# Kernel tuning notes

Measured on AMD Instinct MI355X. Metric: run time of the kernel, lower is better.

Reference implementation:

```python
import jax, jax.numpy as jnp
import numpy as np
from jax.scipy.special import erf, digamma, i0

B, L, D, H = 4, 4096, 512, 4
_MAX_SQRT_GRADIENT = 1000.0

@jax.custom_vjp
def sqrt_bound(x):
    return jnp.sqrt(x)

def _sb_fwd(x):
    return jnp.sqrt(x), x

def _sb_bwd(x, g):
    return (g / jnp.sqrt(jnp.clip(4.0 * x, 1.0 / _MAX_SQRT_GRADIENT**2, None)),)

sqrt_bound.defvjp(_sb_fwd, _sb_bwd)

def block_diag_linear(x, w):
    # x: [..., D], w: [h, bw, bw] block-diagonal weight
    h, bw, _ = w.shape
    xr = x.reshape(x.shape[:-1] + (h, bw))
    return jnp.einsum('...hi,hij->...hj', xr, w).reshape(x.shape)

def self_att_pool(x, num_heads):
    n_state = x.shape[-1] // num_heads
    attn = jax.nn.softmax(jnp.einsum('bld,bmd->blm', x, x) / np.float32(np.sqrt(n_state)), axis=-1)
    # max over the sequence axis of the attended values, keepdims -> [B,1,D]
    return jnp.max(jnp.einsum('blm,bmd->bld', attn, x), axis=-2, keepdims=True)

def ripple_transform_hybrid(t, mix_params):
    mix = jax.nn.softmax(mix_params)
    return mix[0] * digamma(t + 1.0) + mix[1] * i0(t)

def ripple_act(data, alpha, beta, mix_params, temperature=1.0):
    def f(d):
        norm = erf(d / (jnp.max(d) * alpha))
        return jnp.sum(ripple_transform_hybrid(norm * beta, mix_params))
    g = jnp.clip(jax.grad(f)(data), -1.0, 1.0)
    return jax.nn.softmax(-g / temperature, axis=-1)  # softmin

def ripplemoe_act(data, weights, alphas, beta, mix_params, temperature=1.0):
    def f(d):
        dmax = jnp.max(d)
        norm = erf(d[None] / (dmax * alphas[:, None, None]))  # [S,B,L]
        t = ripple_transform_hybrid(norm * beta, mix_params)
        w = jax.nn.softmax(weights)
        return jnp.sum(w[:, None, None] * t)
    g = jnp.clip(jax.grad(f)(data), -1.0, 1.0)
    return jax.nn.softmax(-g / temperature, axis=-1)  # softmin

def token_selection(x, cls_w, cls_b, token_weights, prelu_a, ts_weights, ts_alphas, ts_beta, ts_mix):
    scores = jnp.einsum('bld,sd->sbl', x, cls_w) + cls_b[:, None, None]  # [S,B,L]
    p = jnp.where(scores >= 0, scores, prelu_a * scores)  # PReLU
    ts = jax.nn.celu(p) * jax.nn.silu(p) + jax.nn.gelu(p, approximate=False)
    combined = jnp.einsum('s,sbl->bl', jax.nn.selu(token_weights[:, 0]), ts)
    _, idx = jax.lax.top_k(combined, combined.shape[-1])  # k = L, descending permutation
    vals = ts.sum(0)  # [B,L]
    b_idx = jnp.arange(combined.shape[0])[:, None]
    importance = jnp.ones_like(combined).at[b_idx, idx].add(vals)
    return (1.0 + ripplemoe_act(importance, ts_weights, ts_alphas, ts_beta, ts_mix))[..., None]

def _forward(x, attention_space, W_spatial, W_sil, W_ohead, W_out, w_ig, w_ag, a_param,
             cls_w, cls_b, token_weights, prelu_a, ts_weights, ts_alphas, ts_beta, ts_mix,
             pa1_alpha, pa1_beta, pa1_mix, pa2_alpha, pa2_beta, pa2_mix):
    spatial = jnp.einsum('bld,de->ble', x, attention_space) @ W_spatial.T
    # RG-LRU style gating
    gate_x = jax.nn.sigmoid(block_diag_linear(x, w_ig))
    gate_a = jax.nn.sigmoid(block_diag_linear(x, w_ag))
    log_a = -8.0 * jax.nn.softplus(a_param) * gate_a
    normalized_x = x * gate_x * sqrt_bound(1.0 - jnp.exp(2.0 * log_a))
    gated = jnp.exp(log_a) * self_att_pool(spatial, H) + normalized_x
    sparsity = ripple_act(gated @ W_sil.T, pa1_alpha, pa1_beta, pa1_mix)
    attn = (gated * sparsity) @ W_ohead.T
    sel = token_selection(x, cls_w, cls_b, token_weights, prelu_a, ts_weights, ts_alphas, ts_beta, ts_mix)
    out = ripple_act(attn * sel, pa2_alpha, pa2_beta, pa2_mix)
    return out @ W_out.T

def setup_inputs() -> dict:
    key = jax.random.key(0)
    ks = jax.random.split(key, 12)
    lim = float(1.0 / np.sqrt(D))
    xav = float(np.sqrt(6.0 / (2 * D)))
    bw = D // H
    u = jax.random.uniform(ks[8], (D,), jnp.float32, 0.9**2 + 1e-8, 0.999**2 + 1e-8)
    return {
        'x': jax.random.normal(ks[0], (B, L, D), jnp.float32),
        'attention_space': jax.random.uniform(ks[1], (D, D), jnp.float32, -xav, xav),
        'W_spatial': jax.random.uniform(ks[2], (D, D), jnp.float32, -lim, lim),
        'W_sil': jax.random.uniform(ks[3], (D, D), jnp.float32, -lim, lim),
        'W_ohead': jax.random.uniform(ks[4], (D, D), jnp.float32, -lim, lim),
        'W_out': jax.random.uniform(ks[5], (D, D), jnp.float32, -lim, lim),
        'w_ig': jax.random.normal(ks[6], (H, bw, bw), jnp.float32) * np.float32(np.sqrt(1.0 / bw)),
        'w_ag': jax.random.normal(ks[7], (H, bw, bw), jnp.float32) * np.float32(np.sqrt(1.0 / bw)),
        'a_param': jnp.log(jnp.exp(-0.5 * jnp.log(u)) - 1.0),
        'cls_w': jax.random.uniform(ks[9], (H, D), jnp.float32, -lim, lim),
        'cls_b': jax.random.uniform(ks[10], (H,), jnp.float32, -lim, lim),
        'token_weights': jax.random.normal(ks[11], (H, 1), jnp.float32),
        'prelu_a': jnp.array(0.25, jnp.float32),
        'ts_weights': jnp.ones(H, jnp.float32) / H,
        'ts_alphas': jnp.ones(H, jnp.float32),
        'ts_beta': jnp.array(1.0, jnp.float32),
        'ts_mix': jnp.full((2,), 0.5, jnp.float32),
        'pa1_alpha': jnp.array(1.0, jnp.float32),
        'pa1_beta': jnp.array(1.0, jnp.float32),
        'pa1_mix': jnp.full((2,), 0.5, jnp.float32),
        'pa2_alpha': jnp.array(1.0, jnp.float32),
        'pa2_beta': jnp.array(1.0, jnp.float32),
        'pa2_mix': jnp.full((2,), 0.5, jnp.float32),
    }

def reference(x, attention_space, W_spatial, W_sil, W_ohead, W_out, w_ig, w_ag, a_param,
              cls_w, cls_b, token_weights, prelu_a, ts_weights, ts_alphas, ts_beta, ts_mix,
              pa1_alpha, pa1_beta, pa1_mix, pa2_alpha, pa2_beta, pa2_mix):
    return _forward(x, attention_space, W_spatial, W_sil, W_ohead, W_out, w_ig, w_ag, a_param,
                    cls_w, cls_b, token_weights, prelu_a, ts_weights, ts_alphas, ts_beta, ts_mix,
                    pa1_alpha, pa1_beta, pa1_mix, pa2_alpha, pa2_beta, pa2_mix)
```

## Files before the change

kernel.cpp:

```cpp
#include <hip/hip_runtime.h>

typedef unsigned short ushort;
typedef unsigned int uint;
typedef unsigned long long u64;

#define DEV __device__ __forceinline__

typedef __attribute__((ext_vector_type(4))) float f32x4;
typedef __bf16 bf16x8 __attribute__((ext_vector_type(8)));
typedef __attribute__((ext_vector_type(4))) ushort u16x4;
typedef __attribute__((ext_vector_type(8))) ushort u16x8;

static constexpr int B_ = 4, L_ = 4096, D_ = 512;
static constexpr long NE = (long)B_ * L_ * D_;

DEV float b2f(ushort u) { return __uint_as_float(((uint)u) << 16); }
DEV ushort f2b(float f) {
    uint u = __float_as_uint(f);
    uint r = u + 0x7FFFu + ((u >> 16) & 1u);
    return (ushort)(r >> 16);
}
DEV uint mapF(float f) {
    uint b = __float_as_uint(f);
    return (b & 0x80000000u) ? ~b : (b | 0x80000000u);
}
DEV float unmapF(uint u) {
    uint b = (u & 0x80000000u) ? (u & 0x7FFFFFFFu) : ~u;
    return __uint_as_float(b);
}
DEV float rcp_(float x) { return __builtin_amdgcn_rcpf(x); }
DEV float fexp(float x) { return __builtin_amdgcn_exp2f(x * 1.44269504089f); }
DEV float sigm(float x) { return rcp_(1.f + fexp(-x)); }

DEV void gload16(const ushort* g, ushort* l) {
    __builtin_amdgcn_global_load_lds((const __attribute__((address_space(1))) void*)g,
                                     (__attribute__((address_space(3))) void*)l, 16, 0, 0);
}

DEV int xcd_swz(int b, int nwg) {
    int q = nwg >> 3, r = nwg & 7;
    int x = b & 7, i = b >> 3;
    int base = (x < r) ? x * (q + 1) : r * (q + 1) + (x - r) * q;
    return base + i;
}

DEV float trigamma1p(float t) {
    float x = t + 1.f;
    float acc = 0.f;
#pragma unroll
    for (int k = 0; k < 6; k++) { float xx = x + (float)k; acc += rcp_(xx * xx); }
    float y = x + 6.f;
    float iy = rcp_(y), iy2 = iy * iy;
    return acc + iy * (1.f + iy * (0.5f + iy * (0.166666667f + iy2 * (-0.0333333333f + iy2 * 0.0238095238f))));
}
DEV float besselI1(float t) {
    float q = 0.25f * t * t;
    return 0.5f * t * (1.f + q * (0.5f + q * (0.0833333333f + q * (0.00694444444f + q * (3.47222222e-4f + q * 1.15740741e-5f)))));
}
DEV float rippleH(float u, float beta, float mix0, float mix1) {
    float t = beta * erff(u);
    float Tp = mix0 * trigamma1p(t) + mix1 * besselI1(t);
    float ep = 1.12837917f * fexp(-u * u);
    return beta * Tp * ep;
}

DEV void gemm_core(const ushort* __restrict__ A, int lda,
                   const ushort* __restrict__ Bt, int ldb, int K,
                   ushort* __restrict__ Alds, ushort* __restrict__ Blds,
                   f32x4 (&acc)[4][4])
{
    const int tid = threadIdx.x;
    const int lane = tid & 63;
    const int wave = tid >> 6;
    const int wr = wave >> 1, wc = wave & 1;

    const int srow = wave * 16 + (lane >> 2);
    const int skc = (lane & 3) * 8;
    const ushort* Ag0 = A + (size_t)srow * lda + skc;
    const ushort* Ag1 = A + (size_t)(srow + 64) * lda + skc;
    const ushort* Bg0 = Bt + (size_t)srow * ldb + skc;
    const ushort* Bg1 = Bt + (size_t)(srow + 64) * ldb + skc;
    const int wb = wave * 512;

    const int ar = wr * 64 + (lane & 15);
    const int br = wc * 64 + (lane & 15);
    const int kk = (lane >> 4) * 8;

    gload16(Ag0, Alds + wb);
    gload16(Ag1, Alds + 2048 + wb);
    gload16(Bg0, Blds + wb);
    gload16(Bg1, Blds + 2048 + wb);
    __syncthreads();

    int cur = 0;
    for (int k0 = 0; k0 < K; k0 += 32) {
        const int nb = cur ^ 1;
        if (k0 + 32 < K) {
            gload16(Ag0 + k0 + 32, Alds + nb * 4096 + wb);
            gload16(Ag1 + k0 + 32, Alds + nb * 4096 + 2048 + wb);
            gload16(Bg0 + k0 + 32, Blds + nb * 4096 + wb);
            gload16(Bg1 + k0 + 32, Blds + nb * 4096 + 2048 + wb);
        }
        bf16x8 af[4], bfr[4];
#pragma unroll
        for (int mi = 0; mi < 4; mi++) af[mi] = *(const bf16x8*)&Alds[cur * 4096 + (ar + mi * 16) * 32 + kk];
#pragma unroll
        for (int ni = 0; ni < 4; ni++) bfr[ni] = *(const bf16x8*)&Blds[cur * 4096 + (br + ni * 16) * 32 + kk];
#pragma unroll
        for (int mi = 0; mi < 4; mi++)
#pragma unroll
            for (int ni = 0; ni < 4; ni++)
                acc[mi][ni] = __builtin_amdgcn_mfma_f32_16x16x32_bf16(af[mi], bfr[ni], acc[mi][ni], 0, 0, 0);
        __syncthreads();
        cur = nb;
    }
}

template <int MODE, bool DOMAX>
__global__ __launch_bounds__(256, 4) void gemm_bt(
    const ushort* __restrict__ A, int lda,
    const ushort* __restrict__ Bt, int ldb,
    void* __restrict__ Cv, int ldc, int K,
    const float* __restrict__ rowScale, u64* __restrict__ pmax)
{
    __shared__ ushort Alds[2 * 128 * 32];
    __shared__ ushort Blds[2 * 128 * 32];
    const int nwg = gridDim.x * gridDim.y;
    const int s = xcd_swz(blockIdx.y * gridDim.x + blockIdx.x, nwg);
    const int bx = s % gridDim.x, by = s / gridDim.x;
    const int row0 = by * 128, col0 = bx * 128;
    f32x4 acc[4][4] = {};
    gemm_core(A + (size_t)row0 * lda, lda, Bt + (size_t)col0 * ldb, ldb, K, Alds, Blds, acc);

    const int tid = threadIdx.x;
    const int lane = tid & 63;
    const int wave = tid >> 6;
    const int wr = wave >> 1, wc = wave & 1;
    const int ocol = col0 + wc * 64 + (lane & 15);
    u64 lp = 0;
#pragma unroll
    for (int mi = 0; mi < 4; mi++) {
        const int rbase = row0 + wr * 64 + mi * 16 + (lane >> 4) * 4;
#pragma unroll
        for (int j = 0; j < 4; j++) {
            float sc = (MODE == 3) ? rowScale[rbase + j] : 1.f;
#pragma unroll
            for (int ni = 0; ni < 4; ni++) {
                float v = acc[mi][ni][j] * sc;
                int cc = ocol + ni * 16;
                if (MODE == 0) ((float*)Cv)[(size_t)(rbase + j) * ldc + cc] = v;
                else ((ushort*)Cv)[(size_t)(rbase + j) * ldc + cc] = f2b(v);
                if (DOMAX) {
                    uint idx = (uint)((rbase + j) * ldc + cc);
                    u64 p = ((u64)mapF(v) << 32) | (u64)(~idx);
                    lp = (p > lp) ? p : lp;
                }
            }
        }
    }
    if (DOMAX) {
#pragma unroll
        for (int off = 32; off > 0; off >>= 1) {
            u64 o = __shfl_xor(lp, off);
            lp = (o > lp) ? o : lp;
        }
        if (lane == 0) atomicMax(pmax, lp);
    }
}

__global__ __launch_bounds__(512, 1) void gemm256_exp_k(
    const ushort* __restrict__ spP,
    ushort* __restrict__ Sout,
    float* __restrict__ rowsum)
{
    __shared__ ushort Alds[2 * 256 * 64];
    __shared__ ushort Blds[2 * 256 * 64];
    const int z = blockIdx.z;
    const int nwg = gridDim.x * gridDim.y;
    const int s = xcd_swz(blockIdx.y * gridDim.x + blockIdx.x, nwg);
    const int bx = s % gridDim.x, by = s / gridDim.x;
    const int row0 = by * 256, col0 = bx * 256;
    const ushort* A = spP + (size_t)z * (4096 * 512) + (size_t)row0 * 512;
    const ushort* Bt = spP + (size_t)z * (4096 * 512) + (size_t)col0 * 512;

    const int tid = threadIdx.x;
    const int lane = tid & 63;
    const int wave = tid >> 6;
    const int wr = wave >> 2, wc = wave & 3;

    const int lrow = lane >> 3;
    const int lchunk = (lane & 7) ^ lrow;
    const ushort* Asrc = A + (size_t)(wave * 32 + lrow) * 512 + lchunk * 8;
    const ushort* Bsrc = Bt + (size_t)(wave * 32 + lrow) * 512 + lchunk * 8;
    const int wlds = wave * 2048;

    const int ar = wr * 128 + (lane & 15);
    const int br = wc * 64 + (lane & 15);

    f32x4 acc[8][4] = {};

#define STG(kt, bf) do { \
    _Pragma("unroll") \
    for (int c = 0; c < 4; c++) { \
        gload16(Asrc + (size_t)c * 8 * 512 + (kt) * 64, Alds + (bf) * 16384 + wlds + c * 512); \
        gload16(Bsrc + (size_t)c * 8 * 512 + (kt) * 64, Blds + (bf) * 16384 + wlds + c * 512); \
    } } while (0)

    STG(0, 0);

    for (int kt = 0; kt < 8; kt++) {
        const int cb = kt & 1;
        if (kt < 7) STG(kt + 1, cb ^ 1);
        if (kt < 7) asm volatile("s_waitcnt vmcnt(8)" ::: "memory");
        else        asm volatile("s_waitcnt vmcnt(0)" ::: "memory");
        __builtin_amdgcn_s_barrier();
        asm volatile("" ::: "memory");
        __builtin_amdgcn_s_setprio(1);
#pragma unroll
        for (int ks = 0; ks < 2; ks++) {
            const int kc = ((ks * 4 + (lane >> 4)) ^ (lane & 7)) * 8;
            bf16x8 af[8], bfr[4];
#pragma unroll
            for (int mi = 0; mi < 8; mi++) af[mi] = *(const bf16x8*)&Alds[cb * 16384 + (ar + mi * 16) * 64 + kc];
#pragma unroll
            for (int ni = 0; ni < 4; ni++) bfr[ni] = *(const bf16x8*)&Blds[cb * 16384 + (br + ni * 16) * 64 + kc];
#pragma unroll
            for (int mi = 0; mi < 8; mi++)
#pragma unroll
                for (int ni = 0; ni < 4; ni++)
                    acc[mi][ni] = __builtin_amdgcn_mfma_f32_16x16x32_bf16(af[mi], bfr[ni], acc[mi][ni], 0, 0, 0);
        }
        __builtin_amdgcn_s_setprio(0);
        asm volatile("s_waitcnt lgkmcnt(0)" ::: "memory");
        __builtin_amdgcn_s_barrier();
        asm volatile("" ::: "memory");
    }
#undef STG

    ushort* C = Sout + (size_t)z * 16777216;
    float* rs = rowsum + z * 4096;
    const float sc128 = 0.0883883476f;
    const int ocol = col0 + wc * 64 + (lane & 15);
#pragma unroll
    for (int mi = 0; mi < 8; mi++) {
        const int rbase = row0 + wr * 128 + mi * 16 + (lane >> 4) * 4;
#pragma unroll
        for (int j = 0; j < 4; j++) {
            float rsum = 0.f;
#pragma unroll
            for (int ni = 0; ni < 4; ni++) {
                float p = fexp(acc[mi][ni][j] * sc128);
                C[(size_t)(rbase + j) * 4096 + ocol + ni * 16] = f2b(p);
                rsum += p;
            }
#pragma unroll
            for (int off = 1; off < 16; off <<= 1) rsum += __shfl_xor(rsum, off);
            if ((lane & 15) == 0) atomicAdd(&rs[rbase + j], rsum);
        }
    }
}

__global__ __launch_bounds__(256, 4) void pv_split_k(const ushort* __restrict__ P, const ushort* __restrict__ Vt,
                                                     ushort* __restrict__ part)
{
    __shared__ ushort Alds[2 * 128 * 32];
    __shared__ ushort Blds[2 * 128 * 32];
    const int ks = blockIdx.z;
    const int nwg = gridDim.x * gridDim.y;
    const int s = xcd_swz(blockIdx.y * gridDim.x + blockIdx.x, nwg);
    const int bx = s % gridDim.x, by = s / gridDim.x;
    const int row0 = by * 128, col0 = bx * 128;
    f32x4 acc[4][4] = {};
    gemm_core(P + (size_t)row0 * 4096 + ks * 1024, 4096,
              Vt + (size_t)col0 * 4096 + ks * 1024, 4096, 1024, Alds, Blds, acc);

    ushort* C = part + (size_t)ks * 2097152 + (size_t)row0 * 512 + col0;
    const int tid = threadIdx.x;
    const int lane = tid & 63;
    const int wave = tid >> 6;
    const int wr = wave >> 1, wc = wave & 1;
    const int ocol = wc * 64 + (lane & 15);
#pragma unroll
    for (int mi = 0; mi < 4; mi++) {
        const int rl = wr * 64 + mi * 16 + (lane >> 4) * 4;
#pragma unroll
        for (int j = 0; j < 4; j++)
#pragma unroll
            for (int ni = 0; ni < 4; ni++)
                C[(size_t)(rl + j) * 512 + ocol + ni * 16] = f2b(acc[mi][ni][j]);
    }
}

__global__ __launch_bounds__(256) void pool_combine_k(const ushort* __restrict__ part, const float* __restrict__ rs,
                                                      uint* __restrict__ poolU)
{
    const int tid = threadIdx.x;
    const int l0 = blockIdx.x * 32;
    float m0 = -3.4e38f, m1 = -3.4e38f;
    for (int l = 0; l < 32; l++) {
        size_t off = (size_t)(l0 + l) * 512;
        float iv = rcp_(rs[l0 + l]);
        float s0 = 0.f, s1 = 0.f;
#pragma unroll
        for (int ks = 0; ks < 4; ks++) {
            s0 += b2f(part[(size_t)ks * 2097152 + off + tid]);
            s1 += b2f(part[(size_t)ks * 2097152 + off + tid + 256]);
        }
        m0 = fmaxf(m0, s0 * iv); m1 = fmaxf(m1, s1 * iv);
    }
    atomicMax(&poolU[tid], mapF(m0));
    atomicMax(&poolU[tid + 256], mapF(m1));
}

__global__ __launch_bounds__(256, 4) void gate_gemm_k(const ushort* __restrict__ xb,
                                                      const ushort* __restrict__ wigT, const ushort* __restrict__ wagT,
                                                      ushort* __restrict__ gxab, ushort* __restrict__ gaab)
{
    __shared__ ushort Alds[2 * 128 * 32];
    __shared__ ushort Blds[2 * 128 * 32];
    const int which = blockIdx.x;
    const int h = blockIdx.z;
    const ushort* A = xb + (size_t)blockIdx.y * 128 * 512 + h * 128;
    const ushort* W = (which ? wagT : wigT) + (size_t)h * 16384;
    f32x4 acc[4][4] = {};
    gemm_core(A, 512, W, 128, 128, Alds, Blds, acc);

    ushort* C = (which ? gaab : gxab) + (size_t)blockIdx.y * 128 * 512 + h * 128;
    const int tid = threadIdx.x;
    const int lane = tid & 63;
    const int wave = tid >> 6;
    const int wr = wave >> 1, wc = wave & 1;
    const int ocol = wc * 64 + (lane & 15);
#pragma unroll
    for (int mi = 0; mi < 4; mi++) {
        const int rl = wr * 64 + mi * 16 + (lane >> 4) * 4;
#pragma unroll
        for (int j = 0; j < 4; j++)
#pragma unroll
            for (int ni = 0; ni < 4; ni++)
                C[(size_t)(rl + j) * 512 + ocol + ni * 16] = f2b(acc[mi][ni][j]);
    }
}

__global__ void convert_f2b_k(const float* __restrict__ s, ushort* __restrict__ d, long n4) {
    long i = (long)blockIdx.x * blockDim.x + threadIdx.x;
    long st = (long)gridDim.x * blockDim.x;
    for (; i < n4; i += st) {
        f32x4 v = ((const f32x4*)s)[i];
        u16x4 o;
        o[0] = f2b(v[0]); o[1] = f2b(v[1]); o[2] = f2b(v[2]); o[3] = f2b(v[3]);
        ((u16x4*)d)[i] = o;
    }
}

__global__ void convert_w4_k(const float* __restrict__ w0, const float* __restrict__ w1,
                             const float* __restrict__ w2, const float* __restrict__ w3,
                             ushort* __restrict__ dst) {
    const float* srcs[4] = {w0, w1, w2, w3};
    const float* s = srcs[blockIdx.y];
    ushort* d = dst + (size_t)blockIdx.y * 262144;
    int i = blockIdx.x * 256 + threadIdx.x;
    f32x4 v = ((const f32x4*)s)[i];
    u16x4 o;
    o[0] = f2b(v[0]); o[1] = f2b(v[1]); o[2] = f2b(v[2]); o[3] = f2b(v[3]);
    ((u16x4*)d)[i] = o;
}

template <bool SRCF32>
__global__ __launch_bounds__(256) void transpose_to_bf16(const void* __restrict__ srcv, ushort* __restrict__ dst, int R, int C) {
    __shared__ float tile[32][33];
    const int z = blockIdx.z;
    const float* sf = (const float*)srcv + (size_t)z * R * C;
    const ushort* sb = (const ushort*)srcv + (size_t)z * R * C;
    ushort* dz = dst + (size_t)z * R * C;
    const int tx = threadIdx.x & 31, ty = threadIdx.x >> 5;
    const int c = blockIdx.x * 32 + tx;
#pragma unroll
    for (int k = 0; k < 4; k++) {
        const int r = blockIdx.y * 32 + ty + k * 8;
        tile[ty + k * 8][tx] = SRCF32 ? sf[(size_t)r * C + c] : b2f(sb[(size_t)r * C + c]);
    }
    __syncthreads();
#pragma unroll
    for (int k = 0; k < 4; k++) {
        const int dr = blockIdx.x * 32 + ty + k * 8;
        const int dc = blockIdx.y * 32 + tx;
        dz[(size_t)dr * R + dc] = f2b(tile[tx][ty + k * 8]);
    }
}

__global__ __launch_bounds__(256) void transpose_gates_k(const float* __restrict__ wig, const float* __restrict__ wag,
                                                         ushort* __restrict__ wigT, ushort* __restrict__ wagT) {
    __shared__ float tile[32][33];
    const int which = blockIdx.z >> 2, h = blockIdx.z & 3;
    const float* src = (which ? wag : wig) + (size_t)h * 16384;
    ushort* dst = (which ? wagT : wigT) + (size_t)h * 16384;
    const int tx = threadIdx.x & 31, ty = threadIdx.x >> 5;
    const int c = blockIdx.x * 32 + tx;
#pragma unroll
    for (int k = 0; k < 4; k++) {
        const int r = blockIdx.y * 32 + ty + k * 8;
        tile[ty + k * 8][tx] = src[(size_t)r * 128 + c];
    }
    __syncthreads();
#pragma unroll
    for (int k = 0; k < 4; k++) {
        const int dr = blockIdx.x * 32 + ty + k * 8;
        const int dc = blockIdx.y * 32 + tx;
        dst[(size_t)dr * 128 + dc] = f2b(tile[tx][ty + k * 8]);
    }
}

__global__ void init_misc_k(uint* poolU, u64* pmax) {
    int i = blockIdx.x * 256 + threadIdx.x;
    if (i < 2048) poolU[i] = 0u;
    if (i < 4) pmax[i] = 0ull;
}
__global__ void zero_rs_k(float* rs) {
    rs[blockIdx.x * 256 + threadIdx.x] = 0.f;
}
__global__ void sentinel_k(float* o) { o[threadIdx.x] = 1.0e6f; }

__global__ __launch_bounds__(256) void gates_gated_k(const float* __restrict__ x, const ushort* __restrict__ gxab,
                                                     const ushort* __restrict__ gaab, const float* __restrict__ a_param,
                                                     const uint* __restrict__ poolU, ushort* __restrict__ gatedb) {
    __shared__ float sp8[512];
    const int tid = threadIdx.x;
    for (int d = tid; d < 512; d += 256) {
        float a = a_param[d];
        sp8[d] = 8.f * (fmaxf(a, 0.f) + log1pf(expf(-fabsf(a))));
    }
    __syncthreads();
    long i = (long)blockIdx.x * blockDim.x + tid;
    long st = (long)gridDim.x * blockDim.x;
    const long n8 = NE >> 3;
    for (; i < n8; i += st) {
        u16x8 gx8 = ((const u16x8*)gxab)[i];
        u16x8 ga8 = ((const u16x8*)gaab)[i];
        f32x4 x0 = ((const f32x4*)x)[2 * i];
        f32x4 x1 = ((const f32x4*)x)[2 * i + 1];
        long e = i << 3;
        int b = (int)(e >> 21);
        int d0 = (int)(e & 511);
        u16x8 o;
#pragma unroll
        for (int j = 0; j < 8; j++) {
            float xv = (j < 4) ? x0[j] : x1[j - 4];
            float gx = sigm(b2f(gx8[j]));
            float ga = sigm(b2f(ga8[j]));
            float la = -sp8[d0 + j] * ga;
            float ea = fexp(la);
            float nx = xv * gx * sqrtf(fmaxf(1.f - fexp(2.f * la), 0.f));
            float pl = unmapF(poolU[b * 512 + d0 + j]);
            o[j] = f2b(ea * pl + nx);
        }
        ((u16x8*)gatedb)[i] = o;
    }
}

__global__ __launch_bounds__(256) void redmax2_k(const float* __restrict__ bmax, const int* __restrict__ bidx, int n,
                                                 float* __restrict__ outM, int* __restrict__ outI) {
    __shared__ float rv[256];
    __shared__ int ri[256];
    const int tid = threadIdx.x;
    float bv = -3.4e38f; int bi = -1;
    for (int i = tid; i < n; i += 256) {
        float v = bmax[i]; int ix = bidx[i];
        if (ix >= 0 && (bi < 0 || v > bv || (v == bv && ix < bi))) { bv = v; bi = ix; }
    }
    rv[tid] = bv; ri[tid] = bi; __syncthreads();
    for (int s = 128; s > 0; s >>= 1) {
        if (tid < s) {
            float ov = rv[tid + s]; int oi = ri[tid + s];
            if (oi >= 0 && (ri[tid] < 0 || ov > rv[tid] || (ov == rv[tid] && oi < ri[tid]))) { rv[tid] = ov; ri[tid] = oi; }
        }
        __syncthreads();
    }
    if (tid == 0) { outM[0] = rv[0]; outI[0] = ri[0]; }
}

__global__ __launch_bounds__(256) void ripple_g_k(const ushort* __restrict__ d, ushort* __restrict__ gb, float* __restrict__ sspart,
                                                  const u64* __restrict__ pmax, const float* __restrict__ alpha_p,
                                                  const float* __restrict__ beta_p, const float* __restrict__ mix_p) {
    __shared__ float red[256];
    const int tid = threadIdx.x;
    const float M = unmapF((uint)(pmax[0] >> 32));
    const float alpha = alpha_p[0], beta = beta_p[0];
    float m0 = mix_p[0], m1 = mix_p[1];
    float mm = fmaxf(m0, m1);
    float e0 = fexp(m0 - mm), e1 = fexp(m1 - mm);
    float inv = rcp_(e0 + e1);
    float mix0 = e0 * inv, mix1 = e1 * inv;
    const float invMA = rcp_(M * alpha);
    float ss = 0.f;
    long g = (long)blockIdx.x * 256 + tid;
    const long stride = (long)gridDim.x * 256;
    for (long i = g; i < NE; i += stride) {
        float dv = b2f(d[i]);
        float H = rippleH(dv * invMA, beta, mix0, mix1);
        gb[i] = f2b(H * invMA);
        ss += H * dv;
    }
    red[tid] = ss; __syncthreads();
    for (int s = 128; s > 0; s >>= 1) { if (tid < s) red[tid] += red[tid + s]; __syncthreads(); }
    if (tid == 0) sspart[blockIdx.x] = red[0];
}
__global__ __launch_bounds__(256) void redsum2_k(const float* __restrict__ part, int n, float* __restrict__ out) {
    __shared__ float red[256];
    const int tid = threadIdx.x;
    float s = 0.f;
    for (int i = tid; i < n; i += 256) s += part[i];
    red[tid] = s; __syncthreads();
    for (int q = 128; q > 0; q >>= 1) { if (tid < q) red[tid] += red[tid + q]; __syncthreads(); }
    if (tid == 0) out[0] = red[0];
}

template <int GS>
__global__ __launch_bounds__(256) void ripple_softmax_k(const ushort* __restrict__ gb,
                                                        const u64* __restrict__ pmax,
                                                        const float* __restrict__ ssTot, const float* __restrict__ alpha_p,
                                                        const ushort* __restrict__ gatedb, ushort* __restrict__ outb) {
    __shared__ float red[256];
    const int tid = threadIdx.x;
    const float M = unmapF((uint)(pmax[0] >> 32));
    const int amax = (int)(~(uint)(pmax[0] & 0xFFFFFFFFull));
    const float corr = ssTot[0] * rcp_(M * M * alpha_p[0]);
    long base = (long)blockIdx.x * 512;
    float g0 = b2f(gb[base + tid]);
    float g1 = b2f(gb[base + tid + 256]);
    if ((int)(base + tid) == amax) g0 -= corr;
    if ((int)(base + tid + 256) == amax) g1 -= corr;
    g0 = fminf(fmaxf(g0, -1.f), 1.f);
    g1 = fminf(fmaxf(g1, -1.f), 1.f);
    float mn = fminf(g0, g1);
    red[tid] = mn; __syncthreads();
    for (int s = 128; s > 0; s >>= 1) { if (tid < s) red[tid] = fminf(red[tid], red[tid + s]); __syncthreads(); }
    mn = red[0]; __syncthreads();
    float e0 = fexp(mn - g0), e1 = fexp(mn - g1);
    red[tid] = e0 + e1; __syncthreads();
    for (int s = 128; s > 0; s >>= 1) { if (tid < s) red[tid] += red[tid + s]; __syncthreads(); }
    float inv = rcp_(red[0]);
    if (GS) {
        outb[base + tid] = f2b(b2f(gatedb[base + tid]) * (e0 * inv));
        outb[base + tid + 256] = f2b(b2f(gatedb[base + tid + 256]) * (e1 * inv));
    } else {
        outb[base + tid] = f2b(e0 * inv);
        outb[base + tid + 256] = f2b(e1 * inv);
    }
}

__global__ __launch_bounds__(256) void ts1_k(const float* __restrict__ x, const float* __restrict__ cls_w,
                                             const float* __restrict__ cls_b, const float* __restrict__ tw,
                                             const float* __restrict__ prelu_a,
                                             float* __restrict__ combined, float* __restrict__ vals) {
    __shared__ float cw[2048];
    const int tid = threadIdx.x;
    for (int i = tid; i < 2048; i += 256) cw[i] = cls_w[i];
    __syncthreads();
    const int lane = tid & 63, wid = tid >> 6;
    const int row = blockIdx.x * 4 + wid;
    const float* xr = x + (size_t)row * 512 + lane * 8;
    float pa0 = 0, pa1 = 0, pa2 = 0, pa3 = 0;
#pragma unroll
    for (int j = 0; j < 8; j++) {
        float v = xr[j];
        int c = lane * 8 + j;
        pa0 += v * cw[c]; pa1 += v * cw[512 + c]; pa2 += v * cw[1024 + c]; pa3 += v * cw[1536 + c];
    }
#pragma unroll
    for (int o = 32; o > 0; o >>= 1) {
        pa0 += __shfl_down(pa0, o); pa1 += __shfl_down(pa1, o);
        pa2 += __shfl_down(pa2, o); pa3 += __shfl_down(pa3, o);
    }
    if (lane == 0) {
        float a = prelu_a[0];
        float sc[4] = {pa0, pa1, pa2, pa3};
        float comb = 0.f, vsum = 0.f;
#pragma unroll
        for (int s = 0; s < 4; s++) {
            float p = sc[s] + cls_b[s];
            p = (p >= 0.f) ? p : a * p;
            float cel = (p > 0.f) ? p : expm1f(p);
            float sil = p * sigm(p);
            float gel = 0.5f * p * (1.f + erff(p * 0.70710678f));
            float ts = cel * sil + gel;
            float ww = tw[s];
            float se = 1.05070099f * ((ww > 0.f) ? ww : 1.67326324f * expm1f(ww));
            comb += se * ts;
            vsum += ts;
        }
        combined[row] = comb;
        vals[row] = vsum;
    }
}

__global__ __launch_bounds__(256) void ts2a_k(const float* __restrict__ combined, int* __restrict__ rankp) {
    __shared__ float q[512];
    const int b = blockIdx.z;
    const int tid = threadIdx.x;
    const float* cr = combined + b * 4096;
    const int q0 = blockIdx.y * 512;
    for (int i = tid; i < 512; i += 256) q[i] = cr[q0 + i];
    __syncthreads();
    const int p = blockIdx.x * 256 + tid;
    const float cp = cr[p];
    const f32x4* q4 = (const f32x4*)q;
    int rank = 0;
#pragma unroll 8
    for (int i4 = 0; i4 < 128; i4++) {
        f32x4 v = q4[i4];
        int qb = q0 + i4 * 4;
        rank += (v[0] > cp) || (v[0] == cp && (qb + 0) < p);
        rank += (v[1] > cp) || (v[1] == cp && (qb + 1) < p);
        rank += (v[2] > cp) || (v[2] == cp && (qb + 2) < p);
        rank += (v[3] > cp) || (v[3] == cp && (qb + 3) < p);
    }
    rankp[((b * 8 + blockIdx.y) * 4096) + p] = rank;
}

__global__ __launch_bounds__(256) void ts2b_k(const int* __restrict__ rankp, const float* __restrict__ vals,
                                              float* __restrict__ imp, float* __restrict__ bmax, int* __restrict__ bidx) {
    __shared__ float rv[256];
    __shared__ int ri[256];
    const int tid = threadIdx.x;
    const int b = blockIdx.y;
    const int p = blockIdx.x * 256 + tid;
    int rank = 0;
#pragma unroll
    for (int c = 0; c < 8; c++) rank += rankp[((b * 8 + c) * 4096) + p];
    const int gi = b * 4096 + p;
    const float v = 1.f + vals[b * 4096 + rank];
    imp[gi] = v;
    rv[tid] = v; ri[tid] = gi; __syncthreads();
    for (int s = 128; s > 0; s >>= 1) {
        if (tid < s) {
            float ov = rv[tid + s]; int oi = ri[tid + s];
            if (ov > rv[tid] || (ov == rv[tid] && oi < ri[tid])) { rv[tid] = ov; ri[tid] = oi; }
        }
        __syncthreads();
    }
    if (tid == 0) { bmax[b * 16 + blockIdx.x] = rv[0]; bidx[b * 16 + blockIdx.x] = ri[0]; }
}

__global__ __launch_bounds__(256) void moe_g_k(const float* __restrict__ imp, float* __restrict__ gmoe,
                                               float* __restrict__ sspart, const float* __restrict__ scalM,
                                               const float* __restrict__ tsw, const float* __restrict__ tsa,
                                               const float* __restrict__ tsb, const float* __restrict__ tsmix) {
    __shared__ float red[256];
    const int tid = threadIdx.x;
    const float M = scalM[0];
    float w[4], invMA[4], invA[4];
    {
        float wm = fmaxf(fmaxf(tsw[0], tsw[1]), fmaxf(tsw[2], tsw[3]));
        float s = 0.f;
#pragma unroll
        for (int k = 0; k < 4; k++) { w[k] = fexp(tsw[k] - wm); s += w[k]; }
        float si = rcp_(s);
#pragma unroll
        for (int k = 0; k < 4; k++) { w[k] *= si; invMA[k] = rcp_(M * tsa[k]); invA[k] = rcp_(tsa[k]); }
    }
    const float beta = tsb[0];
    float m0 = tsmix[0], m1 = tsmix[1];
    float mm = fmaxf(m0, m1);
    float e0 = fexp(m0 - mm), e1 = fexp(m1 - mm);
    float minv = rcp_(e0 + e1);
    const float mix0 = e0 * minv, mix1 = e1 * minv;

    float ss = 0.f;
    int i = blockIdx.x * 256 + tid;
    const int stride = gridDim.x * 256;
    for (; i < 65536; i += stride) {
        float dv = imp[i];
        float gbv = 0.f;
#pragma unroll
        for (int s = 0; s < 4; s++) {
            float H = rippleH(dv * invMA[s], beta, mix0, mix1);
            gbv += w[s] * H * invMA[s];
            ss += w[s] * H * dv * invA[s];
        }
        gmoe[i] = gbv;
    }
    red[tid] = ss; __syncthreads();
    for (int s = 128; s > 0; s >>= 1) { if (tid < s) red[tid] += red[tid + s]; __syncthreads(); }
    if (tid == 0) sspart[blockIdx.x] = red[0];
}

__global__ __launch_bounds__(256) void moe_sel_k(const float* __restrict__ gmoe, const float* __restrict__ scalM,
                                                 const int* __restrict__ scalI, const float* __restrict__ sspart,
                                                 float* __restrict__ sel) {
    __shared__ float red[256];
    const int tid = threadIdx.x;
    const int b = blockIdx.x;
    const float M = scalM[0];
    const int amax = scalI[0];
    float ssTot = 0.f;
#pragma unroll
    for (int k = 0; k < 64; k++) ssTot += sspart[k];
    const float corr = ssTot * rcp_(M * M);
    float g[16];
    float mn = 3.4e38f;
#pragma unroll
    for (int k = 0; k < 16; k++) {
        int i = b * 4096 + tid + k * 256;
        float v = gmoe[i];
        if (i == amax) v -= corr;
        v = fminf(fmaxf(v, -1.f), 1.f);
        g[k] = v;
        mn = fminf(mn, v);
    }
    red[tid] = mn; __syncthreads();
    for (int s = 128; s > 0; s >>= 1) { if (tid < s) red[tid] = fminf(red[tid], red[tid + s]); __syncthreads(); }
    mn = red[0]; __syncthreads();
    float sum = 0.f;
#pragma unroll
    for (int k = 0; k < 16; k++) { g[k] = fexp(mn - g[k]); sum += g[k]; }
    red[tid] = sum; __syncthreads();
    for (int s = 128; s > 0; s >>= 1) { if (tid < s) red[tid] += red[tid + s]; __syncthreads(); }
    float inv = rcp_(red[0]);
#pragma unroll
    for (int k = 0; k < 16; k++) sel[b * 4096 + tid + k * 256] = 1.f + g[k] * inv;
}

static constexpr size_t OFF_XB    = 0;
static constexpr size_t OFF_TMPB  = 16777216;
static constexpr size_t OFF_SPB   = 33554432;
static constexpr size_t OFF_SPT   = 50331648;
static constexpr size_t OFF_DBUF  = 67108864;
static constexpr size_t OFF_HBUF  = 100663296;
static constexpr size_t OFF_GATB  = 134217728;
static constexpr size_t OFF_NXB   = 150994944;
static constexpr size_t OFF_EAB   = 167772160;
static constexpr size_t OFF_AST   = 184549376;
static constexpr size_t OFF_WSP   = 185073664;
static constexpr size_t OFF_WSIL  = 185597952;
static constexpr size_t OFF_WOH   = 186122240;
static constexpr size_t OFF_WOUT  = 186646528;
static constexpr size_t OFF_WIGT  = 187170816;
static constexpr size_t OFF_WAGT  = 187301888;
static constexpr size_t OFF_POOL  = 187432960;
static constexpr size_t OFF_SCAL  = 187441152;
static constexpr size_t OFF_SCALI = 187441408;
static constexpr size_t OFF_BMAX  = 187441664;
static constexpr size_t OFF_BIDX  = 187449856;
static constexpr size_t OFF_SSP   = 187458048;
static constexpr size_t OFF_COMB  = 187466240;
static constexpr size_t OFF_VALS  = 187728384;
static constexpr size_t OFF_IMP   = 187990528;
static constexpr size_t OFF_GMOE  = 188252672;
static constexpr size_t OFF_SEL   = 188514816;
static constexpr size_t WS_NEED   = 188776960;

extern "C" void kernel_launch(void* const* d_in, const int* in_sizes, int n_in,
                              void* d_out, int out_size, void* d_ws, size_t ws_size,
                              hipStream_t stream)
{
    (void)in_sizes; (void)n_in; (void)out_size;
    const float* x    = (const float*)d_in[0];
    const float* AS   = (const float*)d_in[1];
    const float* Wsp  = (const float*)d_in[2];
    const float* Wsil = (const float*)d_in[3];
    const float* Woh  = (const float*)d_in[4];
    const float* Wout = (const float*)d_in[5];
    const float* wig  = (const float*)d_in[6];
    const float* wag  = (const float*)d_in[7];
    const float* a_param = (const float*)d_in[8];
    const float* cls_w = (const float*)d_in[9];
    const float* cls_b = (const float*)d_in[10];
    const float* tokw  = (const float*)d_in[11];
    const float* prelu = (const float*)d_in[12];
    const float* tsw   = (const float*)d_in[13];
    const float* tsa   = (const float*)d_in[14];
    const float* tsb   = (const float*)d_in[15];
    const float* tsmix = (const float*)d_in[16];
    const float* p1a = (const float*)d_in[17];
    const float* p1b = (const float*)d_in[18];
    const float* p1m = (const float*)d_in[19];
    const float* p2a = (const float*)d_in[20];
    const float* p2b = (const float*)d_in[21];
    const float* p2m = (const float*)d_in[22];
    float* out = (float*)d_out;

    char* w = (char*)d_ws;
    if (ws_size < WS_NEED) { sentinel_k<<<1, 256, 0, stream>>>(out); return; }

    ushort* xb    = (ushort*)(w + OFF_XB);
    ushort* tmpb  = (ushort*)(w + OFF_TMPB);
    ushort* spb   = (ushort*)(w + OFF_SPB);
    ushort* spT   = (ushort*)(w + OFF_SPT);
    ushort* db    = (ushort*)(w + OFF_DBUF);
    ushort* gbb   = (ushort*)(w + OFF_HBUF);
    ushort* Spair = (ushort*)(w + OFF_DBUF);
    ushort* pvpart= (ushort*)(w + OFF_XB);
    int*    rankp = (int*)(w + OFF_DBUF);
    ushort* gatedb= (ushort*)(w + OFF_GATB);
    ushort* gxab  = (ushort*)(w + OFF_NXB);
    ushort* gaab  = (ushort*)(w + OFF_EAB);
    ushort* ASt   = (ushort*)(w + OFF_AST);
    ushort* Wspb  = (ushort*)(w + OFF_WSP);
    ushort* Wsilb = (ushort*)(w + OFF_WSIL);
    ushort* Wohb  = (ushort*)(w + OFF_WOH);
    ushort* Woutb = (ushort*)(w + OFF_WOUT);
    ushort* wigT  = (ushort*)(w + OFF_WIGT);
    ushort* wagT  = (ushort*)(w + OFF_WAGT);
    uint*   poolU = (uint*)(w + OFF_POOL);
    float*  scal  = (float*)(w + OFF_SCAL);
    u64*    pmax  = (u64*)(w + OFF_SCAL + 128);
    int*    scalI = (int*)(w + OFF_SCALI);
    float*  bmax  = (float*)(w + OFF_BMAX);
    int*    bidx  = (int*)(w + OFF_BIDX);
    float*  sspart= (float*)(w + OFF_SSP);
    float*  comb  = (float*)(w + OFF_COMB);
    float*  rowsum= comb;
    float*  vals  = (float*)(w + OFF_VALS);
    float*  imp   = (float*)(w + OFF_IMP);
    float*  gmoe  = (float*)(w + OFF_GMOE);
    float*  sel   = (float*)(w + OFF_SEL);
    ushort* gsb     = tmpb;
    ushort* probs2b = xb;

    convert_f2b_k<<<2048, 256, 0, stream>>>(x, xb, NE >> 2);
    convert_w4_k<<<dim3(256, 4), 256, 0, stream>>>(Wsp, Wsil, Woh, Wout, Wspb);
    transpose_to_bf16<true><<<dim3(16, 16, 1), 256, 0, stream>>>(AS, ASt, 512, 512);
    transpose_gates_k<<<dim3(4, 4, 8), 256, 0, stream>>>(wig, wag, wigT, wagT);
    init_misc_k<<<8, 256, 0, stream>>>(poolU, pmax);

    gate_gemm_k<<<dim3(2, 128, 4), 256, 0, stream>>>(xb, wigT, wagT, gxab, gaab);

    gemm_bt<1, false><<<dim3(4, 128), 256, 0, stream>>>(xb, 512, ASt, 512, tmpb, 512, 512, nullptr, nullptr);
    gemm_bt<1, false><<<dim3(4, 128), 256, 0, stream>>>(tmpb, 512, Wspb, 512, spb, 512, 512, nullptr, nullptr);

    transpose_to_bf16<false><<<dim3(16, 128, 4), 256, 0, stream>>>(spb, spT, 4096, 512);
    for (int p = 0; p < 2; p++) {
        const ushort* spP = spb + (size_t)(2 * p) * L_ * D_;
        zero_rs_k<<<32, 256, 0, stream>>>(rowsum);
        gemm256_exp_k<<<dim3(16, 16, 2), 512, 0, stream>>>(spP, Spair, rowsum);
        for (int z = 0; z < 2; z++) {
            const int b = 2 * p + z;
            pv_split_k<<<dim3(4, 32, 4), 256, 0, stream>>>(Spair + (size_t)z * 16777216,
                                                           spT + (size_t)b * D_ * L_, pvpart);
            pool_combine_k<<<128, 256, 0, stream>>>(pvpart, rowsum + z * 4096, poolU + b * 512);
        }
    }

    gates_gated_k<<<1024, 256, 0, stream>>>(x, gxab, gaab, a_param, poolU, gatedb);

    gemm_bt<1, true><<<dim3(4, 128), 256, 0, stream>>>(gatedb, 512, Wsilb, 512, db, 512, 512, nullptr, &pmax[0]);
    ripple_g_k<<<2048, 256, 0, stream>>>(db, gbb, sspart, &pmax[0], p1a, p1b, p1m);
    redsum2_k<<<1, 256, 0, stream>>>(sspart, 2048, &scal[1]);
    ripple_softmax_k<1><<<16384, 256, 0, stream>>>(gbb, &pmax[0], &scal[1], p1a, gatedb, gsb);

    ts1_k<<<4096, 256, 0, stream>>>(x, cls_w, cls_b, tokw, prelu, comb, vals);
    ts2a_k<<<dim3(16, 8, 4), 256, 0, stream>>>(comb, rankp);
    ts2b_k<<<dim3(16, 4), 256, 0, stream>>>(rankp, vals, imp, bmax, bidx);
    redmax2_k<<<1, 256, 0, stream>>>(bmax, bidx, 64, &scal[4], &scalI[2]);
    moe_g_k<<<64, 256, 0, stream>>>(imp, gmoe, sspart, &scal[4], tsw, tsa, tsb, tsmix);
    moe_sel_k<<<4, 256, 0, stream>>>(gmoe, &scal[4], &scalI[2], sspart, sel);

    gemm_bt<3, true><<<dim3(4, 128), 256, 0, stream>>>(gsb, 512, Wohb, 512, db, 512, 512, sel, &pmax[1]);

    ripple_g_k<<<2048, 256, 0, stream>>>(db, gbb, sspart, &pmax[1], p2a, p2b, p2m);
    redsum2_k<<<1, 256, 0, stream>>>(sspart, 2048, &scal[3]);
    ripple_softmax_k<0><<<16384, 256, 0, stream>>>(gbb, &pmax[1], &scal[3], p2a, nullptr, probs2b);

    gemm_bt<0, false><<<dim3(4, 128), 256, 0, stream>>>(probs2b, 512, Woutb, 512, out, 512, 512, nullptr, nullptr);
}
```

Before: 598.1 us.

## Merge small kernels and batch per-batch attention launches to cut launch count

Fuses the gate GEMMs and the first xb·ASt GEMM into one 1536-block launch. Folds the buffer zeroing into the weight-conversion kernel and the scalar argmax reduction into its consumer kernels. The PV split-K and pool-combine kernels are each batched over the two batch items of a pair, so the grids get bigger. This removes about ten tiny launches and their serialization gaps, in exchange for larger scratch indexing (pvpart now spans eight slices) and a small amount of redundant per-block reduction work.

```diff
diff --git a/kernel.cpp b/kernel.cpp
--- a/kernel.cpp
+++ b/kernel.cpp
@@ -113,6 +113,23 @@
                 acc[mi][ni] = __builtin_amdgcn_mfma_f32_16x16x32_bf16(af[mi], bfr[ni], acc[mi][ni], 0, 0, 0);
         __syncthreads();
         cur = nb;
+    }
+}
+
+DEV void write_tile_b16(ushort* Cbase, int ldc, f32x4 (&acc)[4][4]) {
+    const int tid = threadIdx.x;
+    const int lane = tid & 63;
+    const int wave = tid >> 6;
+    const int wr = wave >> 1, wc = wave & 1;
+    const int ocol = wc * 64 + (lane & 15);
+#pragma unroll
+    for (int mi = 0; mi < 4; mi++) {
+        const int rl = wr * 64 + mi * 16 + (lane >> 4) * 4;
+#pragma unroll
+        for (int j = 0; j < 4; j++)
+#pragma unroll
+            for (int ni = 0; ni < 4; ni++)
+                Cbase[(size_t)(rl + j) * ldc + ocol + ni * 16] = f2b(acc[mi][ni][j]);
     }
 }
 
@@ -168,6 +185,28 @@
     }
 }
 
+__global__ __launch_bounds__(256, 4) void g1gate_k(
+    const ushort* __restrict__ xb, const ushort* __restrict__ ASt, ushort* __restrict__ tmpb,
+    const ushort* __restrict__ wigT, const ushort* __restrict__ wagT,
+    ushort* __restrict__ gxab, ushort* __restrict__ gaab)
+{
+    __shared__ ushort Alds[2 * 128 * 32];
+    __shared__ ushort Blds[2 * 128 * 32];
+    const int flat = xcd_swz(blockIdx.x, 1536);
+    f32x4 acc[4][4] = {};
+    if (flat < 512) {
+        const int bx = flat & 3, by = flat >> 2;
+        gemm_core(xb + (size_t)(by * 128) * 512, 512, ASt + (size_t)(bx * 128) * 512, 512, 512, Alds, Blds, acc);
+        write_tile_b16(tmpb + (size_t)(by * 128) * 512 + bx * 128, 512, acc);
+    } else {
+        const int f2 = flat - 512;
+        const int which = f2 & 1, row = (f2 >> 1) & 127, h = f2 >> 8;
+        gemm_core(xb + (size_t)row * 128 * 512 + h * 128, 512,
+                  (which ? wagT : wigT) + (size_t)h * 16384, 128, 128, Alds, Blds, acc);
+        write_tile_b16((which ? gaab : gxab) + (size_t)row * 128 * 512 + h * 128, 512, acc);
+    }
+}
+
 __global__ __launch_bounds__(512, 1) void gemm256_exp_k(
     const ushort* __restrict__ spP,
     ushort* __restrict__ Sout,
@@ -260,12 +299,14 @@
     }
 }
 
-__global__ __launch_bounds__(256, 4) void pv_split_k(const ushort* __restrict__ P, const ushort* __restrict__ Vt,
+__global__ __launch_bounds__(256, 4) void pv_split_k(const ushort* __restrict__ Spair, const ushort* __restrict__ VtBase,
                                                      ushort* __restrict__ part)
 {
     __shared__ ushort Alds[2 * 128 * 32];
     __shared__ ushort Blds[2 * 128 * 32];
-    const int ks = blockIdx.z;
+    const int zb = blockIdx.z >> 2, ks = blockIdx.z & 3;
+    const ushort* P = Spair + (size_t)zb * 16777216;
+    const ushort* Vt = VtBase + (size_t)zb * (512 * 4096);
     const int nwg = gridDim.x * gridDim.y;
     const int s = xcd_swz(blockIdx.y * gridDim.x + blockIdx.x, nwg);
     const int bx = s % gridDim.x, by = s / gridDim.x;
@@ -274,26 +315,16 @@
     gemm_core(P + (size_t)row0 * 4096 + ks * 1024, 4096,
               Vt + (size_t)col0 * 4096 + ks * 1024, 4096, 1024, Alds, Blds, acc);
 
-    ushort* C = part + (size_t)ks * 2097152 + (size_t)row0 * 512 + col0;
-    const int tid = threadIdx.x;
-    const int lane = tid & 63;
-    const int wave = tid >> 6;
-    const int wr = wave >> 1, wc = wave & 1;
-    const int ocol = wc * 64 + (lane & 15);
-#pragma unroll
-    for (int mi = 0; mi < 4; mi++) {
-        const int rl = wr * 64 + mi * 16 + (lane >> 4) * 4;
-#pragma unroll
-        for (int j = 0; j < 4; j++)
-#pragma unroll
-            for (int ni = 0; ni < 4; ni++)
-                C[(size_t)(rl + j) * 512 + ocol + ni * 16] = f2b(acc[mi][ni][j]);
-    }
-}
-
-__global__ __launch_bounds__(256) void pool_combine_k(const ushort* __restrict__ part, const float* __restrict__ rs,
-                                                      uint* __restrict__ poolU)
+    write_tile_b16(part + (size_t)blockIdx.z * 2097152 + (size_t)row0 * 512 + col0, 512, acc);
+}
+
+__global__ __launch_bounds__(256) void pool_combine_k(const ushort* __restrict__ partB, const float* __restrict__ rsB,
+                                                      uint* __restrict__ poolB)
 {
+    const int zb = blockIdx.y;
+    const ushort* part = partB + (size_t)zb * 4 * 2097152;
+    const float* rs = rsB + zb * 4096;
+    uint* poolU = poolB + zb * 512;
     const int tid = threadIdx.x;
     const int l0 = blockIdx.x * 32;
     float m0 = -3.4e38f, m1 = -3.4e38f;
@@ -310,36 +341,6 @@
     }
     atomicMax(&poolU[tid], mapF(m0));
     atomicMax(&poolU[tid + 256], mapF(m1));
-}
-
-__global__ __launch_bounds__(256, 4) void gate_gemm_k(const ushort* __restrict__ xb,
-                                                      const ushort* __restrict__ wigT, const ushort* __restrict__ wagT,
-                                                      ushort* __restrict__ gxab, ushort* __restrict__ gaab)
-{
-    __shared__ ushort Alds[2 * 128 * 32];
-    __shared__ ushort Blds[2 * 128 * 32];
-    const int which = blockIdx.x;
-    const int h = blockIdx.z;
-    const ushort* A = xb + (size_t)blockIdx.y * 128 * 512 + h * 128;
-    const ushort* W = (which ? wagT : wigT) + (size_t)h * 16384;
-    f32x4 acc[4][4] = {};
-    gemm_core(A, 512, W, 128, 128, Alds, Blds, acc);
-
-    ushort* C = (which ? gaab : gxab) + (size_t)blockIdx.y * 128 * 512 + h * 128;
-    const int tid = threadIdx.x;
-    const int lane = tid & 63;
-    const int wave = tid >> 6;
-    const int wr = wave >> 1, wc = wave & 1;
-    const int ocol = wc * 64 + (lane & 15);
-#pragma unroll
-    for (int mi = 0; mi < 4; mi++) {
-        const int rl = wr * 64 + mi * 16 + (lane >> 4) * 4;
-#pragma unroll
-        for (int j = 0; j < 4; j++)
-#pragma unroll
-            for (int ni = 0; ni < 4; ni++)
-                C[(size_t)(rl + j) * 512 + ocol + ni * 16] = f2b(acc[mi][ni][j]);
-    }
 }
 
 __global__ void convert_f2b_k(const float* __restrict__ s, ushort* __restrict__ d, long n4) {
@@ -355,7 +356,8 @@
 
 __global__ void convert_w4_k(const float* __restrict__ w0, const float* __restrict__ w1,
                              const float* __restrict__ w2, const float* __restrict__ w3,
-                             ushort* __restrict__ dst) {
+                             ushort* __restrict__ dst,
+                             uint* __restrict__ poolU, u64* __restrict__ pmax, float* __restrict__ rowsum) {
     const float* srcs[4] = {w0, w1, w2, w3};
     const float* s = srcs[blockIdx.y];
     ushort* d = dst + (size_t)blockIdx.y * 262144;
@@ -364,6 +366,16 @@
     u16x4 o;
     o[0] = f2b(v[0]); o[1] = f2b(v[1]); o[2] = f2b(v[2]); o[3] = f2b(v[3]);
     ((u16x4*)d)[i] = o;
+    if (blockIdx.y == 0) {
+        const int x = blockIdx.x;
+        if (x < 32) {
+            rowsum[x * 512 + threadIdx.x] = 0.f;
+            rowsum[x * 512 + 256 + threadIdx.x] = 0.f;
+        } else if (x == 32) {
+            for (int k = threadIdx.x; k < 2048; k += 256) poolU[k] = 0u;
+            if (threadIdx.x < 4) pmax[threadIdx.x] = 0ull;
+        }
+    }
 }
 
 template <bool SRCF32>
@@ -411,14 +423,6 @@
     }
 }
 
-__global__ void init_misc_k(uint* poolU, u64* pmax) {
-    int i = blockIdx.x * 256 + threadIdx.x;
-    if (i < 2048) poolU[i] = 0u;
-    if (i < 4) pmax[i] = 0ull;
-}
-__global__ void zero_rs_k(float* rs) {
-    rs[blockIdx.x * 256 + threadIdx.x] = 0.f;
-}
 __global__ void sentinel_k(float* o) { o[threadIdx.x] = 1.0e6f; }
 
 __global__ __launch_bounds__(256) void gates_gated_k(const float* __restrict__ x, const ushort* __restrict__ gxab,
@@ -456,27 +460,6 @@
         }
         ((u16x8*)gatedb)[i] = o;
     }
-}
-
-__global__ __launch_bounds__(256) void redmax2_k(const float* __restrict__ bmax, const int* __restrict__ bidx, int n,
-                                                 float* __restrict__ outM, int* __restrict__ outI) {
-    __shared__ float rv[256];
-    __shared__ int ri[256];
-    const int tid = threadIdx.x;
-    float bv = -3.4e38f; int bi = -1;
-    for (int i = tid; i < n; i += 256) {
-        float v = bmax[i]; int ix = bidx[i];
-        if (ix >= 0 && (bi < 0 || v > bv || (v == bv && ix < bi))) { bv = v; bi = ix; }
-    }
-    rv[tid] = bv; ri[tid] = bi; __syncthreads();
-    for (int s = 128; s > 0; s >>= 1) {
-        if (tid < s) {
-            float ov = rv[tid + s]; int oi = ri[tid + s];
-            if (oi >= 0 && (ri[tid] < 0 || ov > rv[tid] || (ov == rv[tid] && oi < ri[tid]))) { rv[tid] = ov; ri[tid] = oi; }
-        }
-        __syncthreads();
-    }
-    if (tid == 0) { outM[0] = rv[0]; outI[0] = ri[0]; }
 }
 
 __global__ __launch_bounds__(256) void ripple_g_k(const ushort* __restrict__ d, ushort* __restrict__ gb, float* __restrict__ sspart,
@@ -643,12 +626,14 @@
 }
 
 __global__ __launch_bounds__(256) void moe_g_k(const float* __restrict__ imp, float* __restrict__ gmoe,
-                                               float* __restrict__ sspart, const float* __restrict__ scalM,
+                                               float* __restrict__ sspart, const float* __restrict__ bmax,
                                                const float* __restrict__ tsw, const float* __restrict__ tsa,
                                                const float* __restrict__ tsb, const float* __restrict__ tsmix) {
     __shared__ float red[256];
     const int tid = threadIdx.x;
-    const float M = scalM[0];
+    float M = -3.4e38f;
+#pragma unroll
+    for (int k = 0; k < 64; k++) M = fmaxf(M, bmax[k]);
     float w[4], invMA[4], invA[4];
     {
         float wm = fmaxf(fmaxf(tsw[0], tsw[1]), fmaxf(tsw[2], tsw[3]));
@@ -685,14 +670,18 @@
     if (tid == 0) sspart[blockIdx.x] = red[0];
 }
 
-__global__ __launch_bounds__(256) void moe_sel_k(const float* __restrict__ gmoe, const float* __restrict__ scalM,
-                                                 const int* __restrict__ scalI, const float* __restrict__ sspart,
+__global__ __launch_bounds__(256) void moe_sel_k(const float* __restrict__ gmoe, const float* __restrict__ bmax,
+                                                 const int* __restrict__ bidx, const float* __restrict__ sspart,
                                                  float* __restrict__ sel) {
     __shared__ float red[256];
     const int tid = threadIdx.x;
     const int b = blockIdx.x;
-    const float M = scalM[0];
-    const int amax = scalI[0];
+    float M = -3.4e38f; int amax = 0x7FFFFFFF;
+#pragma unroll
+    for (int k = 0; k < 64; k++) {
+        float v = bmax[k]; int ix = bidx[k];
+        if (v > M || (v == M && ix < amax)) { M = v; amax = ix; }
+    }
     float ssTot = 0.f;
 #pragma unroll
     for (int k = 0; k < 64; k++) ssTot += sspart[k];
@@ -805,7 +794,6 @@
     uint*   poolU = (uint*)(w + OFF_POOL);
     float*  scal  = (float*)(w + OFF_SCAL);
     u64*    pmax  = (u64*)(w + OFF_SCAL + 128);
-    int*    scalI = (int*)(w + OFF_SCALI);
     float*  bmax  = (float*)(w + OFF_BMAX);
     int*    bidx  = (int*)(w + OFF_BIDX);
     float*  sspart= (float*)(w + OFF_SSP);
@@ -819,27 +807,20 @@
     ushort* probs2b = xb;
 
     convert_f2b_k<<<2048, 256, 0, stream>>>(x, xb, NE >> 2);
-    convert_w4_k<<<dim3(256, 4), 256, 0, stream>>>(Wsp, Wsil, Woh, Wout, Wspb);
+    convert_w4_k<<<dim3(256, 4), 256, 0, stream>>>(Wsp, Wsil, Woh, Wout, Wspb, poolU, pmax, rowsum);
     transpose_to_bf16<true><<<dim3(16, 16, 1), 256, 0, stream>>>(AS, ASt, 512, 512);
     transpose_gates_k<<<dim3(4, 4, 8), 256, 0, stream>>>(wig, wag, wigT, wagT);
-    init_misc_k<<<8, 256, 0, stream>>>(poolU, pmax);
-
-    gate_gemm_k<<<dim3(2, 128, 4), 256, 0, stream>>>(xb, wigT, wagT, gxab, gaab);
-
-    gemm_bt<1, false><<<dim3(4, 128), 256, 0, stream>>>(xb, 512, ASt, 512, tmpb, 512, 512, nullptr, nullptr);
+
+    g1gate_k<<<1536, 256, 0, stream>>>(xb, ASt, tmpb, wigT, wagT, gxab, gaab);
+
     gemm_bt<1, false><<<dim3(4, 128), 256, 0, stream>>>(tmpb, 512, Wspb, 512, spb, 512, 512, nullptr, nullptr);
 
     transpose_to_bf16<false><<<dim3(16, 128, 4), 256, 0, stream>>>(spb, spT, 4096, 512);
     for (int p = 0; p < 2; p++) {
         const ushort* spP = spb + (size_t)(2 * p) * L_ * D_;
-        zero_rs_k<<<32, 256, 0, stream>>>(rowsum);
-        gemm256_exp_k<<<dim3(16, 16, 2), 512, 0, stream>>>(spP, Spair, rowsum);
-        for (int z = 0; z < 2; z++) {
-            const int b = 2 * p + z;
-            pv_split_k<<<dim3(4, 32, 4), 256, 0, stream>>>(Spair + (size_t)z * 16777216,
-                                                           spT + (size_t)b * D_ * L_, pvpart);
-            pool_combine_k<<<128, 256, 0, stream>>>(pvpart, rowsum + z * 4096, poolU + b * 512);
-        }
+        gemm256_exp_k<<<dim3(16, 16, 2), 512, 0, stream>>>(spP, Spair, rowsum + p * 8192);
+        pv_split_k<<<dim3(4, 32, 8), 256, 0, stream>>>(Spair, spT + (size_t)(2 * p) * D_ * L_, pvpart);
+        pool_combine_k<<<dim3(128, 2), 256, 0, stream>>>(pvpart, rowsum + p * 8192, poolU + 2 * p * 512);
     }
 
     gates_gated_k<<<1024, 256, 0, stream>>>(x, gxab, gaab, a_param, poolU, gatedb);
@@ -852,9 +833,8 @@
     ts1_k<<<4096, 256, 0, stream>>>(x, cls_w, cls_b, tokw, prelu, comb, vals);
     ts2a_k<<<dim3(16, 8, 4), 256, 0, stream>>>(comb, rankp);
     ts2b_k<<<dim3(16, 4), 256, 0, stream>>>(rankp, vals, imp, bmax, bidx);
-    redmax2_k<<<1, 256, 0, stream>>>(bmax, bidx, 64, &scal[4], &scalI[2]);
-    moe_g_k<<<64, 256, 0, stream>>>(imp, gmoe, sspart, &scal[4], tsw, tsa, tsb, tsmix);
-    moe_sel_k<<<4, 256, 0, stream>>>(gmoe, &scal[4], &scalI[2], sspart, sel);
+    moe_g_k<<<64, 256, 0, stream>>>(imp, gmoe, sspart, bmax, tsw, tsa, tsb, tsmix);
+    moe_sel_k<<<4, 256, 0, stream>>>(gmoe, bmax, bidx, sspart, sel);
 
     gemm_bt<3, true><<<dim3(4, 128), 256, 0, stream>>>(gsb, 512, Wohb, 512, db, 512, 512, sel, &pmax[1]);
 
```

New measurement: 561.1 us. -6.2%, faster.
